# Performance work log

Measured on AMD Instinct MI355X. Metric: run time of the kernel, lower is better.

## Reference

```python
import jax, jax.numpy as jnp
import numpy as np

V = 5023          # FLAME vertex count
NJ = 5            # joints: global, neck, jaw, eyeL, eyeR
N_SHAPE = 100
N_EXP = 50
PARENTS = np.array([-1, 0, 1, 1, 1], dtype=np.int64)  # static kintree
N_BATCH = 2048


def setup_inputs() -> dict:
    key = jax.random.key(0)
    ks = jax.random.split(key, 12)
    N = N_BATCH
    shape = jax.random.normal(ks[0], (N, N_SHAPE), jnp.float32)
    exp = jax.random.normal(ks[1], (N, N_EXP), jnp.float32)
    neck_pose = 0.1 * jax.random.normal(ks[2], (N, 3), jnp.float32)
    jaw_pose = 0.1 * jax.random.normal(ks[3], (N, 3), jnp.float32)
    eye_pose = 0.1 * jax.random.normal(ks[4], (N, 6), jnp.float32)
    v_template = jax.random.normal(ks[5], (V, 3), jnp.float32)
    shapedirs = 0.01 * jax.random.normal(ks[6], (V, 3, N_SHAPE + N_EXP), jnp.float32)
    posedirs = 0.01 * jax.random.normal(ks[7], (36, V * 3), jnp.float32)
    J_regressor = jax.random.uniform(ks[8], (NJ, V), jnp.float32)
    J_regressor = J_regressor / J_regressor.sum(axis=1, keepdims=True)
    lbs_weights = jax.random.uniform(ks[9], (V, NJ), jnp.float32)
    lbs_weights = lbs_weights / lbs_weights.sum(axis=1, keepdims=True)
    parents = jnp.asarray(PARENTS)
    return dict(shape=shape, exp=exp, neck_pose=neck_pose, jaw_pose=jaw_pose,
                eye_pose=eye_pose, v_template=v_template, shapedirs=shapedirs,
                posedirs=posedirs, J_regressor=J_regressor, lbs_weights=lbs_weights,
                parents=parents)


def rodrigues(rot_vecs):
    """Axis-angle [...,3] -> rotation matrices [...,3,3] (matches SMPL/FLAME impl)."""
    angle = jnp.linalg.norm(rot_vecs + 1e-8, axis=-1, keepdims=True)
    rd = rot_vecs / angle
    cos = jnp.cos(angle)[..., None]
    sin = jnp.sin(angle)[..., None]
    rx, ry, rz = rd[..., 0], rd[..., 1], rd[..., 2]
    z = jnp.zeros_like(rx)
    K = jnp.stack([z, -rz, ry, rz, z, -rx, -ry, rx, z], axis=-1).reshape(rd.shape + (3,))
    I = jnp.eye(3, dtype=rot_vecs.dtype)
    return I + sin * K + (1.0 - cos) * (K @ K)


def flame_forward(shape, exp, neck_pose, jaw_pose, eye_pose, v_template,
                  shapedirs, posedirs, J_regressor, lbs_weights):
    N = shape.shape[0]
    dt = shape.dtype
    betas = jnp.concatenate([shape, exp], axis=1)                      # [N,150]
    # full pose: zeroed global rot + neck + jaw + eyes -> [N,NJ,3]
    full_pose = jnp.concatenate([jnp.zeros_like(jaw_pose), neck_pose,
                                 jaw_pose, eye_pose], axis=1).reshape(N, NJ, 3)
    # shape blendshapes
    v_shaped = v_template[None] + jnp.einsum('bl,vkl->bvk', betas, shapedirs)  # [N,V,3]
    J = jnp.einsum('jv,bvk->bjk', J_regressor, v_shaped)               # [N,NJ,3]
    # pose blendshapes
    R = rodrigues(full_pose)                                           # [N,NJ,3,3]
    pose_feature = (R[:, 1:] - jnp.eye(3, dtype=dt)).reshape(N, (NJ - 1) * 9)
    v_posed = v_shaped + (pose_feature @ posedirs).reshape(N, V, 3)
    # kinematic chain (static 5-joint tree)
    rel_J = J.at[:, 1:].add(-J[:, PARENTS[1:]])
    Rt = jnp.concatenate([R, rel_J[..., None]], axis=-1)               # [N,NJ,3,4]
    bottom = jnp.broadcast_to(jnp.array([0., 0., 0., 1.], dtype=dt), (N, NJ, 1, 4))
    T = jnp.concatenate([Rt, bottom], axis=2)                          # [N,NJ,4,4]
    chain = [T[:, 0]]
    for i in range(1, NJ):
        chain.append(chain[int(PARENTS[i])] @ T[:, i])
    G = jnp.stack(chain, axis=1)                                       # [N,NJ,4,4]
    # remove rest-pose joint locations from the transforms
    J_h = jnp.concatenate([J, jnp.zeros((N, NJ, 1), dt)], axis=-1)     # [N,NJ,4]
    t_corr = jnp.einsum('bjrc,bjc->bjr', G, J_h)
    A = G.at[..., 3].add(-t_corr)                                      # [N,NJ,4,4]
    # linear blend skinning
    Tw = jnp.einsum('vj,bjrc->bvrc', lbs_weights, A)                   # [N,V,4,4]
    v_h = jnp.concatenate([v_posed, jnp.ones((N, V, 1), dt)], axis=-1)
    verts = jnp.einsum('bvrc,bvc->bvr', Tw, v_h)[..., :3]              # [N,V,3]
    return verts


def reference(shape, exp, neck_pose, jaw_pose, eye_pose, v_template,
              shapedirs, posedirs, J_regressor, lbs_weights, parents):
    # parents is a static buffer (PARENTS) -- accepted for signature parity.
    return flame_forward(shape, exp, neck_pose, jaw_pose, eye_pose, v_template,
                         shapedirs, posedirs, J_regressor, lbs_weights)
```

## Files before the change

kernel.cpp:

```cpp
#include <hip/hip_runtime.h>
#include <hip/hip_bf16.h>
#include <math.h>

#define NV   5023
#define N3   15069
#define NB   2048
#define NTIL 79
#define NPAD (NTIL*192)

#define WS_JD_B   0
#define WS_ATR_B  9216
#define WS_AB_B   795648
#define WS_BB_B   1582080

#define GP_J 126
#define GP_S 1067
#define GP_P 237

typedef __attribute__((ext_vector_type(8))) short short8;
typedef __attribute__((ext_vector_type(4))) float floatx4;

static __device__ __forceinline__ unsigned short f2bf(float x) {
    union { __hip_bfloat16 h; unsigned short s; } u;
    u.h = __float2bfloat16(x);
    return u.s;
}
static __device__ __forceinline__ unsigned int pk2(float a, float b) {
    return (unsigned int)f2bf(a) | ((unsigned int)f2bf(b) << 16);
}

#define BAR_LGKM() do { \
    asm volatile("s_waitcnt lgkmcnt(0)" ::: "memory"); \
    __builtin_amdgcn_s_barrier(); \
    asm volatile("" ::: "memory"); \
} while (0)

__global__ void k_prep(const float* __restrict__ Jreg,
                       const float* __restrict__ sdirs,
                       const float* __restrict__ vt,
                       const float* __restrict__ pdirs,
                       char* __restrict__ ws) {
    __shared__ float JregL[200];
    __shared__ float PL[36][65];
    const int t = threadIdx.x;

    if (blockIdx.x < GP_J) {
        int slice = blockIdx.x;
        int start = slice * 40;
        int end   = min(start + 40, NV);
        if (t < 200) {
            int j = t / 40, vl = t % 40;
            int v = start + vl;
            JregL[t] = (v < NV) ? Jreg[j * NV + v] : 0.f;
        }
        __syncthreads();
        int s0 = t, s1 = t + 256;
        float a0[5] = {0,0,0,0,0}, a1[5] = {0,0,0,0,0};
        #pragma unroll 2
        for (int v = start; v < end; ++v) {
            int vl = v - start;
            float x0 = (s0 < 450) ? sdirs[(size_t)v * 450 + s0]
                     : (s0 < 453 ? vt[v * 3 + (s0 - 450)] : 0.f);
            float x1 = (s1 < 450) ? sdirs[(size_t)v * 450 + s1]
                     : (s1 < 453 ? vt[v * 3 + (s1 - 450)] : 0.f);
            #pragma unroll
            for (int j = 0; j < 5; ++j) {
                float w = JregL[j * 40 + vl];
                a0[j] += w * x0; a1[j] += w * x1;
            }
        }
        float* Jd = (float*)(ws + WS_JD_B);
        #pragma unroll
        for (int j = 0; j < 5; ++j) {
            if (s0 < 453) atomicAdd(&Jd[j * 453 + s0], a0[j]);
            if (s1 < 453) atomicAdd(&Jd[j * 453 + s1], a1[j]);
        }
    } else if (blockIdx.x < GP_J + GP_S) {
        int idx = (blockIdx.x - GP_J) * 256 + t;
        if (idx < NPAD * 18) {
            int n = idx / 18, g = idx % 18;
            __hip_bfloat16* dst = (__hip_bfloat16*)(ws + WS_BB_B) + (size_t)n * 192 + g * 8;
            if (n < N3) {
                const float* src = sdirs + (size_t)n * 150 + g * 8;
                float2 p0 = *(const float2*)(src);
                float2 p1 = *(const float2*)(src + 2);
                float2 p2 = *(const float2*)(src + 4);
                float2 p3 = *(const float2*)(src + 6);
                unsigned int w[4] = { pk2(p0.x, p0.y), pk2(p1.x, p1.y),
                                      pk2(p2.x, p2.y), pk2(p3.x, p3.y) };
                *(int4*)dst = *(int4*)w;
            } else {
                int4 z = {0, 0, 0, 0};
                *(int4*)dst = z;
            }
        }
    } else {
        int pb = blockIdx.x - (GP_J + GP_S);
        int n0 = pb * 64;
        #pragma unroll
        for (int j = 0; j < 9; ++j) {
            int flat = j * 256 + t;
            int k = flat >> 6, i = flat & 63;
            int n = n0 + i;
            PL[k][i] = (n < N3) ? pdirs[(size_t)k * N3 + n] : 0.f;
        }
        __syncthreads();
        #pragma unroll
        for (int j = 0; j < 2; ++j) {
            int idx2 = j * 256 + t;
            if (idx2 < 384) {
                int r = idx2 / 6, g = idx2 % 6;
                int n = n0 + r;
                int k0 = 144 + g * 8;
                __hip_bfloat16 val[8];
                #pragma unroll
                for (int e = 0; e < 8; ++e) {
                    int k = k0 + e;
                    float v = 0.f;
                    if (k < 150)      v = (n < N3) ? sdirs[(size_t)n * 150 + k] : 0.f;
                    else if (k < 186) v = PL[k - 150][r];
                    val[e] = __float2bfloat16(v);
                }
                *(int4*)((__hip_bfloat16*)(ws + WS_BB_B) + (size_t)n * 192 + k0) = *(int4*)val;
            }
        }
    }
}

static __device__ __forceinline__ void rodr3(float rx, float ry, float rz, float* R) {
    float ax = rx + 1e-8f, ay = ry + 1e-8f, az = rz + 1e-8f;
    float angle = sqrtf(ax*ax + ay*ay + az*az);
    float inv = 1.f / angle;
    float ux = rx * inv, uy = ry * inv, uz = rz * inv;
    float c = cosf(angle), s = sinf(angle);
    float K[9] = {0.f, -uz, uy,  uz, 0.f, -ux,  -uy, ux, 0.f};
    float KK[9];
    #pragma unroll
    for (int r = 0; r < 3; ++r)
        #pragma unroll
        for (int cc = 0; cc < 3; ++cc) {
            float a = 0.f;
            #pragma unroll
            for (int m = 0; m < 3; ++m) a += K[r*3+m] * K[m*3+cc];
            KK[r*3+cc] = a;
        }
    #pragma unroll
    for (int e = 0; e < 9; ++e) R[e] = s * K[e] + (1.f - c) * KK[e];
    R[0] += 1.f; R[4] += 1.f; R[8] += 1.f;
}

__global__ void k_batch(const float* __restrict__ shp,
                        const float* __restrict__ expn,
                        const float* __restrict__ neck,
                        const float* __restrict__ jaw,
                        const float* __restrict__ eye,
                        char* __restrict__ ws) {
    __shared__ float JdL[2265];
    {
        const float* Jd = (const float*)(ws + WS_JD_B);
        for (int i = threadIdx.x; i < 2265; i += 64) JdL[i] = Jd[i];
    }
    __syncthreads();
    int b = blockIdx.x * 64 + threadIdx.x;
    float* Atr = (float*)(ws + WS_ATR_B) + (size_t)b * 60;
    unsigned int* A32 = (unsigned int*)((char*)ws + WS_AB_B + (size_t)b * 384);

    float J[15];
    #pragma unroll
    for (int jk = 0; jk < 15; ++jk) J[jk] = JdL[(jk / 3) * 453 + 450 + (jk % 3)];

    for (int l4 = 0; l4 < 25; ++l4) {
        float4 be = *(const float4*)(shp + (size_t)b * 100 + l4 * 4);
        A32[2*l4]     = pk2(be.x, be.y);
        A32[2*l4 + 1] = pk2(be.z, be.w);
        float bev[4] = {be.x, be.y, be.z, be.w};
        #pragma unroll
        for (int e = 0; e < 4; ++e) {
            int l = l4 * 4 + e;
            #pragma unroll
            for (int jj = 0; jj < 5; ++jj)
                #pragma unroll
                for (int kk = 0; kk < 3; ++kk)
                    J[jj * 3 + kk] += JdL[jj * 453 + kk * 150 + l] * bev[e];
        }
    }
    for (int l2 = 0; l2 < 25; ++l2) {
        float2 be = *(const float2*)(expn + (size_t)b * 50 + l2 * 2);
        A32[50 + l2] = pk2(be.x, be.y);
        float bev[2] = {be.x, be.y};
        #pragma unroll
        for (int e = 0; e < 2; ++e) {
            int l = 100 + l2 * 2 + e;
            #pragma unroll
            for (int jj = 0; jj < 5; ++jj)
                #pragma unroll
                for (int kk = 0; kk < 3; ++kk)
                    J[jj * 3 + kk] += JdL[jj * 453 + kk * 150 + l] * bev[e];
        }
    }

    float R[4][9];
    rodr3(neck[b*3], neck[b*3+1], neck[b*3+2], R[0]);
    rodr3(jaw[b*3],  jaw[b*3+1],  jaw[b*3+2],  R[1]);
    rodr3(eye[b*6],  eye[b*6+1],  eye[b*6+2],  R[2]);
    rodr3(eye[b*6+3], eye[b*6+4], eye[b*6+5],  R[3]);

    #pragma unroll
    for (int i = 0; i < 18; ++i) {
        int x0 = 2*i, x1 = 2*i + 1;
        float p0 = R[x0/9][x0%9] - (((x0%9) % 4) == 0 ? 1.f : 0.f);
        float p1 = R[x1/9][x1%9] - (((x1%9) % 4) == 0 ? 1.f : 0.f);
        A32[75 + i] = pk2(p0, p1);
    }
    A32[93] = 0u; A32[94] = 0u; A32[95] = 0u;

    Atr[0]=1.f; Atr[1]=0.f; Atr[2]=0.f;  Atr[3]=0.f;
    Atr[4]=0.f; Atr[5]=1.f; Atr[6]=0.f;  Atr[7]=0.f;
    Atr[8]=0.f; Atr[9]=0.f; Atr[10]=1.f; Atr[11]=0.f;
    #pragma unroll
    for (int r = 0; r < 3; ++r) {
        float d = R[0][r*3+0]*J[3] + R[0][r*3+1]*J[4] + R[0][r*3+2]*J[5];
        Atr[12 + r*4 + 0] = R[0][r*3+0];
        Atr[12 + r*4 + 1] = R[0][r*3+1];
        Atr[12 + r*4 + 2] = R[0][r*3+2];
        Atr[12 + r*4 + 3] = J[3+r] - d;
    }
    #pragma unroll
    for (int kk = 1; kk < 4; ++kk) {
        int jj = kk + 1;
        float rel[3];
        #pragma unroll
        for (int r = 0; r < 3; ++r) rel[r] = J[jj*3+r] - J[3+r];
        float Gr[9], tv[3];
        #pragma unroll
        for (int r = 0; r < 3; ++r) {
            #pragma unroll
            for (int cc = 0; cc < 3; ++cc) {
                float a = 0.f;
                #pragma unroll
                for (int m = 0; m < 3; ++m) a += R[0][r*3+m] * R[kk][m*3+cc];
                Gr[r*3+cc] = a;
            }
            tv[r] = R[0][r*3+0]*rel[0] + R[0][r*3+1]*rel[1] + R[0][r*3+2]*rel[2] + J[3+r];
        }
        #pragma unroll
        for (int r = 0; r < 3; ++r) {
            float d = Gr[r*3+0]*J[jj*3+0] + Gr[r*3+1]*J[jj*3+1] + Gr[r*3+2]*J[jj*3+2];
            Atr[jj*12 + r*4 + 0] = Gr[r*3+0];
            Atr[jj*12 + r*4 + 1] = Gr[r*3+1];
            Atr[jj*12 + r*4 + 2] = Gr[r*3+2];
            Atr[jj*12 + r*4 + 3] = tv[r] - d;
        }
    }
}

#define A_OFF  0
#define B_OFF  8704
#define S_VT   33
#define S_AT   61
#define VT_T_OFF 0
#define ATR_OFF  25344
#define VTQ_OFF  33152
#define LBS_OFF  33920
#define SMEM_BYTES 35200

__global__ __launch_bounds__(256, 3) void k_mega(
        const char* __restrict__ ws,
        const float* __restrict__ vt,
        const float* __restrict__ lbsw,
        float* __restrict__ out) {
    __shared__ __align__(16) unsigned char smem[SMEM_BYTES];
    const unsigned char* AbG = (const unsigned char*)ws + WS_AB_B;
    const unsigned char* BbG = (const unsigned char*)ws + WS_BB_B;
    const float* AtrG = (const float*)(ws + WS_ATR_B);

    const int ntile = blockIdx.y;
    const int b0    = blockIdx.x * 64;
    const int t     = threadIdx.x;
    const int lane  = t & 63;
    const int wn    = t >> 6;
    const int l15 = lane & 15, quad = lane >> 4;

    floatx4 acc[4][3];
    #pragma unroll
    for (int f = 0; f < 4; ++f)
        #pragma unroll
        for (int g = 0; g < 3; ++g) {
            floatx4 z = {0.f, 0.f, 0.f, 0.f};
            acc[f][g] = z;
        }

    for (int chunk = 0; chunk < 3; ++chunk) {
        __syncthreads();
        #pragma unroll
        for (int i = 0; i < 2; ++i) {
            int flat = i * 256 + t;
            int row = flat >> 3, piece = flat & 7;
            *(float4*)(smem + A_OFF + row * 136 + piece * 16) =
                *(const float4*)(AbG + (size_t)(b0 + row) * 384 + chunk * 128 + piece * 16);
        }
        #pragma unroll
        for (int i = 0; i < 6; ++i) {
            int flat = i * 256 + t;
            int row = flat >> 3, piece = flat & 7;
            *(float4*)(smem + B_OFF + row * 136 + piece * 16) =
                *(const float4*)(BbG + (size_t)(ntile * 192 + row) * 384 + chunk * 128 + piece * 16);
        }
        __syncthreads();
        #pragma unroll
        for (int ks = 0; ks < 2; ++ks) {
            short8 af[4];
            #pragma unroll
            for (int f = 0; f < 4; ++f)
                af[f] = *(const short8*)(smem + A_OFF + (f * 16 + l15) * 136 + ks * 64 + quad * 16);
            #pragma unroll
            for (int g = 0; g < 3; ++g) {
                short8 bf = *(const short8*)(smem + B_OFF + (wn * 48 + g * 16 + l15) * 136 + ks * 64 + quad * 16);
                #pragma unroll
                for (int f = 0; f < 4; ++f)
                    acc[f][g] = __builtin_amdgcn_mfma_f32_16x16x32_bf16(af[f], bf, acc[f][g], 0, 0, 0);
            }
        }
    }
    __syncthreads();

    float* vtT  = (float*)(smem + VT_T_OFF);
    float* atrS = (float*)(smem + ATR_OFF);
    float* vtQ  = (float*)(smem + VTQ_OFF);
    float* lbsS = (float*)(smem + LBS_OFF);

    if (t < 192) { int n = ntile * 192 + t; vtQ[t] = (n < N3) ? vt[n] : 0.f; }
    for (int i = t; i < 320; i += 256) {
        int v = ntile * 64 + i / 5;
        lbsS[i] = (v < NV) ? lbsw[(size_t)v * 5 + (i % 5)] : 0.f;
    }
    float arA[8], arB[8];
    #pragma unroll
    for (int u = 0; u < 8; ++u) {
        int i = u * 256 + t;
        arA[u] = (i < 1920) ? AtrG[(size_t)b0 * 60 + i] : 0.f;
    }

    #define EPI_PHASE(QQ, ARCUR, PRELOAD_NEXT)                                          \
    {                                                                                   \
        BAR_LGKM();                                                                     \
                                   \
        _Pragma("unroll")                                                               \
        for (int ff2 = 0; ff2 < 2; ++ff2) {                                             \
            int f = QQ * 2 + ff2;                                                       \
            _Pragma("unroll")                                                           \
            for (int g = 0; g < 3; ++g) {                                               \
                int col = wn * 48 + g * 16 + l15;                                       \
                int rl  = ff2 * 16 + quad * 4;                                          \
                _Pragma("unroll")                                                       \
                for (int r = 0; r < 4; ++r)                                             \
                    vtT[col * S_VT + rl + r] = acc[f][g][r];                            \
            }                                                                           \
        }                                                                               \
                                                         \
        _Pragma("unroll")                                                               \
        for (int u = 0; u < 8; ++u) {                                                   \
            int i = u * 256 + t;                                                        \
            if (i < 1920) {                                                             \
                int rw = i / 60, cw = i - rw * 60;                                      \
                atrS[rw * S_AT + cw] = ARCUR[u];                                        \
            }                                                                           \
        }                                                                               \
        PRELOAD_NEXT                                                                    \
        BAR_LGKM();                                                                     \
                                        \
        {                                                                               \
            int rl = t & 31;                                                            \
            int vgrp = t >> 5;                                                          \
            float ar[60];                                                               \
            _Pragma("unroll")                                                           \
            for (int i = 0; i < 60; ++i) ar[i] = atrS[rl * S_AT + i];                   \
            _Pragma("unroll")                                                           \
            for (int vv = 0; vv < 8; ++vv) {                                            \
                int vloc = vgrp * 8 + vv;                                               \
                int c0 = vloc * 3;                                                      \
                float w0 = lbsS[vloc*5+0], w1 = lbsS[vloc*5+1], w2 = lbsS[vloc*5+2],    \
                      w3 = lbsS[vloc*5+3], w4 = lbsS[vloc*5+4];                         \
                float px = vtT[(c0+0) * S_VT + rl] + vtQ[c0+0];                         \
                float py = vtT[(c0+1) * S_VT + rl] + vtQ[c0+1];                         \
                float pz = vtT[(c0+2) * S_VT + rl] + vtQ[c0+2];                         \
                float y[3];                                                             \
                _Pragma("unroll")                                                       \
                for (int r = 0; r < 3; ++r) {                                           \
                    float t0 = w0*ar[ 0+r*4+0] + w1*ar[12+r*4+0] + w2*ar[24+r*4+0]      \
                             + w3*ar[36+r*4+0] + w4*ar[48+r*4+0];                       \
                    float t1 = w0*ar[ 0+r*4+1] + w1*ar[12+r*4+1] + w2*ar[24+r*4+1]      \
                             + w3*ar[36+r*4+1] + w4*ar[48+r*4+1];                       \
                    float t2 = w0*ar[ 0+r*4+2] + w1*ar[12+r*4+2] + w2*ar[24+r*4+2]      \
                             + w3*ar[36+r*4+2] + w4*ar[48+r*4+2];                       \
                    float t3 = w0*ar[ 0+r*4+3] + w1*ar[12+r*4+3] + w2*ar[24+r*4+3]      \
                             + w3*ar[36+r*4+3] + w4*ar[48+r*4+3];                       \
                    y[r] = t0*px + t1*py + t2*pz + t3;                                  \
                }                                                                       \
                vtT[(c0+0) * S_VT + rl] = y[0];                                         \
                vtT[(c0+1) * S_VT + rl] = y[1];                                         \
                vtT[(c0+2) * S_VT + rl] = y[2];                                         \
            }                                                                           \
        }                                                                               \
        BAR_LGKM();                                                                     \
                  \
        {                                                                               \
            int wv = t >> 6;                                                            \
            const bool full = (ntile * 192 + 192 <= N3);                                \
            for (int rr = wv; rr < 32; rr += 4) {                                       \
                size_t ob = (size_t)(b0 + QQ * 32 + rr) * N3 + (size_t)ntile * 192;     \
                if (full) {                                                             \
                    _Pragma("unroll")                                                   \
                    for (int e = 0; e < 3; ++e) {                                       \
                        int col = e * 64 + lane;                                        \
                        out[ob + col] = vtT[col * S_VT + rr];                           \
                    }                                                                   \
                } else {                                                                \
                    _Pragma("unroll")                                                   \
                    for (int e = 0; e < 3; ++e) {                                       \
                        int col = e * 64 + lane;                                        \
                        if (ntile * 192 + col < N3)                                     \
                            out[ob + col] = vtT[col * S_VT + rr];                       \
                    }                                                                   \
                }                                                                       \
            }                                                                           \
        }                                                                               \
    }

    EPI_PHASE(0, arA,
        { _Pragma("unroll")
          for (int u = 0; u < 8; ++u) {
              int i = u * 256 + t;
              arB[u] = (i < 1920) ? AtrG[(size_t)(b0 + 32) * 60 + i] : 0.f;
          } } )
    EPI_PHASE(1, arB, { } )
    #undef EPI_PHASE
}

extern "C" void kernel_launch(void* const* d_in, const int* in_sizes, int n_in,
                              void* d_out, int out_size, void* d_ws, size_t ws_size,
                              hipStream_t stream) {
    const float* shp  = (const float*)d_in[0];
    const float* expn = (const float*)d_in[1];
    const float* neck = (const float*)d_in[2];
    const float* jaw  = (const float*)d_in[3];
    const float* eye  = (const float*)d_in[4];
    const float* vt   = (const float*)d_in[5];
    const float* sdir = (const float*)d_in[6];
    const float* pdir = (const float*)d_in[7];
    const float* jreg = (const float*)d_in[8];
    const float* lbsw = (const float*)d_in[9];
    char* ws  = (char*)d_ws;
    float* out = (float*)d_out;

    hipMemsetAsync(ws + WS_JD_B, 0, 2272 * 4, stream);
    k_prep <<<GP_J + GP_S + GP_P, 256, 0, stream>>>(jreg, sdir, vt, pdir, ws);
    k_batch<<<32, 64, 0, stream>>>(shp, expn, neck, jaw, eye, ws);
    k_mega <<<dim3(32, NTIL), 256, 0, stream>>>(ws, vt, lbsw, out);
}
```

Baseline: 247.6 us.

## Parallelize k_batch over 256 threads with smem staging and coalesced packing

k_batch now uses 256 threads per block. Shape and expression inputs are staged into padded shared memory with coalesced loads, the 150-term joint regression is split across four thread segments and reduced in shared memory, and the bf16 A-matrix rows are written cooperatively with coalesced stores. The aim is to cut the latency of the tiny 32-block kernel, where each thread previously did strided serial loads and scattered stores. k_mega's launch bounds also rise to 4 blocks per CU, which constrains registers and may cause spills.

```diff
diff --git a/kernel.cpp b/kernel.cpp
--- a/kernel.cpp
+++ b/kernel.cpp
@@ -149,108 +149,125 @@
     R[0] += 1.f; R[4] += 1.f; R[8] += 1.f;
 }
 
-__global__ void k_batch(const float* __restrict__ shp,
-                        const float* __restrict__ expn,
-                        const float* __restrict__ neck,
-                        const float* __restrict__ jaw,
-                        const float* __restrict__ eye,
-                        char* __restrict__ ws) {
-    __shared__ float JdL[2265];
+#define KBS 0
+#define KBE 6464
+#define KBJ 9728
+#define KBR 11993
+#define KBP 16345
+#define KBT 18713
+
+__global__ __launch_bounds__(256) void k_batch(
+        const float* __restrict__ shp,
+        const float* __restrict__ expn,
+        const float* __restrict__ neck,
+        const float* __restrict__ jaw,
+        const float* __restrict__ eye,
+        char* __restrict__ ws) {
+    __shared__ float L[KBT];
+    const int t  = threadIdx.x;
+    const int b0 = blockIdx.x * 64;
+
     {
         const float* Jd = (const float*)(ws + WS_JD_B);
-        for (int i = threadIdx.x; i < 2265; i += 64) JdL[i] = Jd[i];
+        for (int i = t; i < 6400; i += 256) { int r = i / 100, c = i - r * 100; L[KBS + r*101 + c] = shp[(size_t)b0*100 + i]; }
+        for (int i = t; i < 3200; i += 256) { int r = i / 50,  c = i - r * 50;  L[KBE + r*51  + c] = expn[(size_t)b0*50 + i]; }
+        for (int i = t; i < 2265; i += 256) L[KBJ + i] = Jd[i];
     }
     __syncthreads();
-    int b = blockIdx.x * 64 + threadIdx.x;
-    float* Atr = (float*)(ws + WS_ATR_B) + (size_t)b * 60;
-    unsigned int* A32 = (unsigned int*)((char*)ws + WS_AB_B + (size_t)b * 384);
-
-    float J[15];
-    #pragma unroll
-    for (int jk = 0; jk < 15; ++jk) J[jk] = JdL[(jk / 3) * 453 + 450 + (jk % 3)];
-
-    for (int l4 = 0; l4 < 25; ++l4) {
-        float4 be = *(const float4*)(shp + (size_t)b * 100 + l4 * 4);
-        A32[2*l4]     = pk2(be.x, be.y);
-        A32[2*l4 + 1] = pk2(be.z, be.w);
-        float bev[4] = {be.x, be.y, be.z, be.w};
-        #pragma unroll
-        for (int e = 0; e < 4; ++e) {
-            int l = l4 * 4 + e;
+
+    const int br = t & 63, seg = t >> 6;
+    {
+        float Jp[15];
+        #pragma unroll
+        for (int u = 0; u < 15; ++u) Jp[u] = 0.f;
+        int l0 = seg * 38, l1 = (seg == 3) ? 150 : (l0 + 38);
+        for (int l = l0; l < l1; ++l) {
+            float be = (l < 100) ? L[KBS + br*101 + l] : L[KBE + br*51 + (l - 100)];
             #pragma unroll
             for (int jj = 0; jj < 5; ++jj)
                 #pragma unroll
                 for (int kk = 0; kk < 3; ++kk)
-                    J[jj * 3 + kk] += JdL[jj * 453 + kk * 150 + l] * bev[e];
-        }
-    }
-    for (int l2 = 0; l2 < 25; ++l2) {
-        float2 be = *(const float2*)(expn + (size_t)b * 50 + l2 * 2);
-        A32[50 + l2] = pk2(be.x, be.y);
-        float bev[2] = {be.x, be.y};
-        #pragma unroll
-        for (int e = 0; e < 2; ++e) {
-            int l = 100 + l2 * 2 + e;
-            #pragma unroll
-            for (int jj = 0; jj < 5; ++jj)
+                    Jp[jj*3 + kk] += L[KBJ + jj*453 + kk*150 + l] * be;
+        }
+        #pragma unroll
+        for (int u = 0; u < 15; ++u) L[KBR + (seg*64 + br)*17 + u] = Jp[u];
+    }
+    __syncthreads();
+
+    if (t < 64) {
+        int b = b0 + t;
+        float J[15];
+        #pragma unroll
+        for (int jk = 0; jk < 15; ++jk) {
+            float s = L[KBJ + (jk/3)*453 + 450 + (jk%3)];
+            #pragma unroll
+            for (int sg = 0; sg < 4; ++sg) s += L[KBR + (sg*64 + t)*17 + jk];
+            J[jk] = s;
+        }
+
+        float R[4][9];
+        rodr3(neck[b*3], neck[b*3+1], neck[b*3+2], R[0]);
+        rodr3(jaw[b*3],  jaw[b*3+1],  jaw[b*3+2],  R[1]);
+        rodr3(eye[b*6],  eye[b*6+1],  eye[b*6+2],  R[2]);
+        rodr3(eye[b*6+3], eye[b*6+4], eye[b*6+5],  R[3]);
+
+        #pragma unroll
+        for (int kk2 = 0; kk2 < 4; ++kk2)
+            #pragma unroll
+            for (int e = 0; e < 9; ++e)
+                L[KBP + t*37 + kk2*9 + e] = R[kk2][e] - ((e == 0 || e == 4 || e == 8) ? 1.f : 0.f);
+
+        float* Atr = (float*)(ws + WS_ATR_B) + (size_t)b * 60;
+        Atr[0]=1.f; Atr[1]=0.f; Atr[2]=0.f;  Atr[3]=0.f;
+        Atr[4]=0.f; Atr[5]=1.f; Atr[6]=0.f;  Atr[7]=0.f;
+        Atr[8]=0.f; Atr[9]=0.f; Atr[10]=1.f; Atr[11]=0.f;
+        #pragma unroll
+        for (int r = 0; r < 3; ++r) {
+            float d = R[0][r*3+0]*J[3] + R[0][r*3+1]*J[4] + R[0][r*3+2]*J[5];
+            Atr[12 + r*4 + 0] = R[0][r*3+0];
+            Atr[12 + r*4 + 1] = R[0][r*3+1];
+            Atr[12 + r*4 + 2] = R[0][r*3+2];
+            Atr[12 + r*4 + 3] = J[3+r] - d;
+        }
+        #pragma unroll
+        for (int kk = 1; kk < 4; ++kk) {
+            int jj = kk + 1;
+            float rel[3];
+            #pragma unroll
+            for (int r = 0; r < 3; ++r) rel[r] = J[jj*3+r] - J[3+r];
+            float Gr[9], tv[3];
+            #pragma unroll
+            for (int r = 0; r < 3; ++r) {
                 #pragma unroll
-                for (int kk = 0; kk < 3; ++kk)
-                    J[jj * 3 + kk] += JdL[jj * 453 + kk * 150 + l] * bev[e];
-        }
-    }
-
-    float R[4][9];
-    rodr3(neck[b*3], neck[b*3+1], neck[b*3+2], R[0]);
-    rodr3(jaw[b*3],  jaw[b*3+1],  jaw[b*3+2],  R[1]);
-    rodr3(eye[b*6],  eye[b*6+1],  eye[b*6+2],  R[2]);
-    rodr3(eye[b*6+3], eye[b*6+4], eye[b*6+5],  R[3]);
-
-    #pragma unroll
-    for (int i = 0; i < 18; ++i) {
-        int x0 = 2*i, x1 = 2*i + 1;
-        float p0 = R[x0/9][x0%9] - (((x0%9) % 4) == 0 ? 1.f : 0.f);
-        float p1 = R[x1/9][x1%9] - (((x1%9) % 4) == 0 ? 1.f : 0.f);
-        A32[75 + i] = pk2(p0, p1);
-    }
-    A32[93] = 0u; A32[94] = 0u; A32[95] = 0u;
-
-    Atr[0]=1.f; Atr[1]=0.f; Atr[2]=0.f;  Atr[3]=0.f;
-    Atr[4]=0.f; Atr[5]=1.f; Atr[6]=0.f;  Atr[7]=0.f;
-    Atr[8]=0.f; Atr[9]=0.f; Atr[10]=1.f; Atr[11]=0.f;
-    #pragma unroll
-    for (int r = 0; r < 3; ++r) {
-        float d = R[0][r*3+0]*J[3] + R[0][r*3+1]*J[4] + R[0][r*3+2]*J[5];
-        Atr[12 + r*4 + 0] = R[0][r*3+0];
-        Atr[12 + r*4 + 1] = R[0][r*3+1];
-        Atr[12 + r*4 + 2] = R[0][r*3+2];
-        Atr[12 + r*4 + 3] = J[3+r] - d;
-    }
-    #pragma unroll
-    for (int kk = 1; kk < 4; ++kk) {
-        int jj = kk + 1;
-        float rel[3];
-        #pragma unroll
-        for (int r = 0; r < 3; ++r) rel[r] = J[jj*3+r] - J[3+r];
-        float Gr[9], tv[3];
-        #pragma unroll
-        for (int r = 0; r < 3; ++r) {
-            #pragma unroll
-            for (int cc = 0; cc < 3; ++cc) {
-                float a = 0.f;
-                #pragma unroll
-                for (int m = 0; m < 3; ++m) a += R[0][r*3+m] * R[kk][m*3+cc];
-                Gr[r*3+cc] = a;
-            }
-            tv[r] = R[0][r*3+0]*rel[0] + R[0][r*3+1]*rel[1] + R[0][r*3+2]*rel[2] + J[3+r];
-        }
-        #pragma unroll
-        for (int r = 0; r < 3; ++r) {
-            float d = Gr[r*3+0]*J[jj*3+0] + Gr[r*3+1]*J[jj*3+1] + Gr[r*3+2]*J[jj*3+2];
-            Atr[jj*12 + r*4 + 0] = Gr[r*3+0];
-            Atr[jj*12 + r*4 + 1] = Gr[r*3+1];
-            Atr[jj*12 + r*4 + 2] = Gr[r*3+2];
-            Atr[jj*12 + r*4 + 3] = tv[r] - d;
-        }
+                for (int cc = 0; cc < 3; ++cc) {
+                    float a = 0.f;
+                    #pragma unroll
+                    for (int m = 0; m < 3; ++m) a += R[0][r*3+m] * R[kk][m*3+cc];
+                    Gr[r*3+cc] = a;
+                }
+                tv[r] = R[0][r*3+0]*rel[0] + R[0][r*3+1]*rel[1] + R[0][r*3+2]*rel[2] + J[3+r];
+            }
+            #pragma unroll
+            for (int r = 0; r < 3; ++r) {
+                float d = Gr[r*3+0]*J[jj*3+0] + Gr[r*3+1]*J[jj*3+1] + Gr[r*3+2]*J[jj*3+2];
+                Atr[jj*12 + r*4 + 0] = Gr[r*3+0];
+                Atr[jj*12 + r*4 + 1] = Gr[r*3+1];
+                Atr[jj*12 + r*4 + 2] = Gr[r*3+2];
+                Atr[jj*12 + r*4 + 3] = tv[r] - d;
+            }
+        }
+    }
+    __syncthreads();
+
+    unsigned int* A32g = (unsigned int*)(ws + WS_AB_B);
+    for (int i = t; i < 6144; i += 256) {
+        int r = i / 96, w = i - r * 96;
+        unsigned int val;
+        if (w < 50)      val = pk2(L[KBS + r*101 + 2*w],     L[KBS + r*101 + 2*w + 1]);
+        else if (w < 75) { int c = 2*(w-50); val = pk2(L[KBE + r*51 + c], L[KBE + r*51 + c + 1]); }
+        else if (w < 93) { int c = 2*(w-75); val = pk2(L[KBP + r*37 + c], L[KBP + r*37 + c + 1]); }
+        else             val = 0u;
+        A32g[(size_t)(b0 + r)*96 + w] = val;
     }
 }
 
@@ -264,7 +281,7 @@
 #define LBS_OFF  33920
 #define SMEM_BYTES 35200
 
-__global__ __launch_bounds__(256, 3) void k_mega(
+__global__ __launch_bounds__(256, 4) void k_mega(
         const char* __restrict__ ws,
         const float* __restrict__ vt,
         const float* __restrict__ lbsw,
@@ -455,6 +472,6 @@
 
     hipMemsetAsync(ws + WS_JD_B, 0, 2272 * 4, stream);
     k_prep <<<GP_J + GP_S + GP_P, 256, 0, stream>>>(jreg, sdir, vt, pdir, ws);
-    k_batch<<<32, 64, 0, stream>>>(shp, expn, neck, jaw, eye, ws);
+    k_batch<<<32, 256, 0, stream>>>(shp, expn, neck, jaw, eye, ws);
     k_mega <<<dim3(32, NTIL), 256, 0, stream>>>(ws, vt, lbsw, out);
 }
```

Measured after the change: 247.3 us. About the same (-0.1%).
